# Performance work log

Hardware: AMD Instinct MI355X
Metric: run time of the kernel (lower is better)

Reference implementation:

```python
import jax, jax.numpy as jnp
import numpy as np

B, T, F, L = 512, 512, 128, 512  # batch, seq_len, n_features, latent_dim


def setup_inputs() -> dict:
    key = jax.random.key(0)
    ks = jax.random.split(key, 8)
    s = 1.0 / np.sqrt(L)  # torch default init scale for GRUCell (hidden_size=L)
    sd = 1.0 / np.sqrt(L)  # torch Linear(L, F) init scale
    return {
        "x": jax.random.normal(ks[0], (B, T, F), jnp.float32),
        "h_0": jax.random.normal(ks[1], (1, B, L), jnp.float32),
        "W_ih": jax.random.uniform(ks[2], (3 * L, F), jnp.float32, -s, s),
        "W_hh": jax.random.uniform(ks[3], (3 * L, L), jnp.float32, -s, s),
        "b_ih": jax.random.uniform(ks[4], (3 * L,), jnp.float32, -s, s),
        "b_hh": jax.random.uniform(ks[5], (3 * L,), jnp.float32, -s, s),
        "Wd": jax.random.uniform(ks[6], (F, L), jnp.float32, -sd, sd),
        "bd": jax.random.uniform(ks[7], (F,), jnp.float32, -sd, sd),
        "seq_len": T,
    }


def reference(x, h_0, W_ih, W_hh, b_ih, b_hh, Wd, bd, seq_len):
    # epsilon=0.0 default: teacher forcing never fires, so x_t = dense(h_t).
    h = jnp.squeeze(h_0, axis=0)          # [B, L]
    xt = h @ Wd.T + bd                    # [B, F]  (initial dense(h_0))

    def step(carry, _):
        h, xt = carry
        gi = xt @ W_ih.T + b_ih           # [B, 3L]
        gh = h @ W_hh.T + b_hh            # [B, 3L]
        i_r, i_z, i_n = jnp.split(gi, 3, axis=-1)
        h_r, h_z, h_n = jnp.split(gh, 3, axis=-1)
        r = jax.nn.sigmoid(i_r + h_r)
        z = jax.nn.sigmoid(i_z + h_z)
        n = jnp.tanh(i_n + r * h_n)
        h_new = (1.0 - z) * n + z * h     # [B, L]
        x_new = h_new @ Wd.T + bd         # [B, F] == dense(h_t) == output[:, t]
        return (h_new, x_new), x_new

    _, ys = jax.lax.scan(step, (h, xt), None, length=seq_len)  # ys: [T, B, F]
    return jnp.transpose(ys, (1, 0, 2))   # [B, T, F]
```

## Files before the change

kernel.cpp:

```cpp
#include <hip/hip_runtime.h>
#include <stdint.h>

typedef _Float16 f16;
typedef _Float16 half8 __attribute__((ext_vector_type(8)));
typedef _Float16 half4 __attribute__((ext_vector_type(4)));
typedef float float4v __attribute__((ext_vector_type(4)));
typedef float float2v __attribute__((ext_vector_type(2)));
typedef unsigned int u32;

#define MFMA16(A, B, C) __builtin_amdgcn_mfma_f32_16x16x32_f16((A), (B), (C), 0, 0, 0)

static constexpr int Bsz = 512, Tsz = 512, Fsz = 128, Lsz = 512;
static constexpr int NPACK = 2176;
static constexpr float LO_S = 2048.0f, LO_R = 1.0f / 2048.0f;

static constexpr size_t WSZ_FRAG  = (size_t)(NPACK / 16) * 16 * 64 * 8 * 2;
static constexpr size_t OFF_WHI   = 0;
static constexpr size_t OFF_WLO   = OFF_WHI + WSZ_FRAG;
static constexpr size_t OFF_BIAS  = OFF_WLO + WSZ_FRAG;
static constexpr size_t OFF_HHI   = OFF_BIAS + 16384;
static constexpr size_t OFF_HLO   = OFF_HHI + (size_t)2 * Bsz * Lsz * 2;
static constexpr size_t OFF_FLAGS = OFF_HLO + (size_t)2 * Bsz * Lsz * 2;

static constexpr int EXS = 37;
static constexpr int LDS_HI = 0;
static constexpr int LDS_LO = 32768;
static constexpr int LDS_EX = 65536;
static constexpr int LDS_YP = LDS_EX + 16 * 32 * EXS * 4;
static constexpr int LDS_TOT = LDS_YP + 4 * 32 * 17 * 4;

__device__ __host__ __forceinline__ int swz(int c, int r) {
  return (((c >> 3) ^ (r & 7)) << 3) | (c & 7);
}

__device__ __forceinline__ void async16(const void* g, void* l) {
  __builtin_amdgcn_global_load_lds((const __attribute__((address_space(1))) u32*)g,
                                   (__attribute__((address_space(3))) u32*)l, 16, 0, 16);
}

__device__ __forceinline__ float sigm(float x) { return 1.0f / (1.0f + __expf(-x)); }
__device__ __forceinline__ float tanh_(float x) { return 1.0f - 2.0f / (__expf(2.0f * x) + 1.0f); }

__global__ void k_pack(const float* __restrict__ Wih, const float* __restrict__ Whh,
                       const float* __restrict__ Wd, f16* __restrict__ whiF,
                       f16* __restrict__ wloF) {
  const int c = blockIdx.y;
  const int l = blockIdx.x * 256 + threadIdx.x;
  float v;
  if (c < 1536) {
    const float* wih = Wih + c * 128;
    float acc = 0.f;
#pragma unroll 8
    for (int f = 0; f < 128; ++f) acc = fmaf(Wd[f * 512 + l], wih[f], acc);
    v = acc;
    if (c < 1024) v += Whh[c * 512 + l];
  } else if (c < 2048) {
    v = Whh[(c - 512) * 512 + l];
  } else {
    v = Wd[(c - 2048) * 512 + l];
  }
  f16 hi = (f16)v;
  f16 lo = (f16)((v - (float)hi) * LO_S);
  const int chunk = c >> 4, ks = l >> 5, q = (l >> 3) & 3, j = l & 7, n = c & 15;
  const size_t idx = (((size_t)(chunk * 16 + ks)) * 64 + q * 16 + n) * 8 + j;
  whiF[idx] = hi;
  wloF[idx] = lo;
}

__global__ void k_init(const float* __restrict__ h0, const float* __restrict__ Wih,
                       const float* __restrict__ bih, const float* __restrict__ bhh,
                       const float* __restrict__ bd, f16* __restrict__ hhi,
                       f16* __restrict__ hlo, float* __restrict__ biasP,
                       int* __restrict__ flags) {
  const int t = blockIdx.x * 256 + threadIdx.x;
  if (t < Bsz * Lsz) {
    const int row = t >> 9, col = t & 511;
    float v = h0[t];
    f16 hi = (f16)v;
    f16 lo = (f16)((v - (float)hi) * LO_S);
    const int cp = swz(col, row);
    hhi[row * 512 + cp] = hi;
    hlo[row * 512 + cp] = lo;
  }
  if (t < NPACK) {
    float v;
    if (t < 1536) {
      float a = bih[t];
      for (int f = 0; f < 128; ++f) a = fmaf(Wih[t * 128 + f], bd[f], a);
      if (t < 1024) a += bhh[t];
      v = a;
    } else if (t < 2048) {
      v = bhh[t - 512];
    } else {
      v = bd[t - 2048];
    }
    biasP[t] = v;
  }
  if (t < 8192) flags[t] = 0;
}

__global__ __launch_bounds__(256, 1) void k_main(
    const float* __restrict__ h0, const f16* __restrict__ whiF,
    const f16* __restrict__ wloF, const float* __restrict__ biasP,
    f16* __restrict__ hhi, f16* __restrict__ hlo, int* __restrict__ flags,
    float* __restrict__ out) {
  extern __shared__ char dsm[];
  f16* sHi = (f16*)(dsm + LDS_HI);
  f16* sLo = (f16*)(dsm + LDS_LO);
  float* ex = (float*)(dsm + LDS_EX);
  float* yp = (float*)(dsm + LDS_YP);

  const int bid = blockIdx.x;
  const int g = bid & 15;
  const int m = bid >> 4;
  const int tid = threadIdx.x;
  const int v = tid >> 6, lane = tid & 63, q = lane >> 4, n = lane & 15;

  const half8* whiV = (const half8*)whiF;
  const half8* wloV = (const half8*)wloF;
  half8 w_hi[4][2][4], w_lo[4][2][4];
#pragma unroll
  for (int t = 0; t < 4; ++t)
#pragma unroll
    for (int nt = 0; nt < 2; ++nt)
#pragma unroll
      for (int ks = 0; ks < 4; ++ks) {
        const int idx = ((t * 32 + m * 2 + nt) * 16 + v * 4 + ks) * 64 + lane;
        w_hi[t][nt][ks] = whiV[idx];
        w_lo[t][nt][ks] = wloV[idx];
      }
  half8 w_y[4];
  if (m < 8) {
#pragma unroll
    for (int ks = 0; ks < 4; ++ks) w_y[ks] = whiV[((128 + m) * 16 + v * 4 + ks) * 64 + lane];
  }

  const int rl = tid >> 3, c0 = (tid & 7) * 4;
  float bias[4][4];
#pragma unroll
  for (int t = 0; t < 4; ++t)
#pragma unroll
    for (int cc = 0; cc < 4; ++cc) bias[t][cc] = biasP[t * 512 + m * 32 + c0 + cc];
  float hreg[4];
#pragma unroll
  for (int cc = 0; cc < 4; ++cc)
    hreg[cc] = h0[(size_t)(32 * g + rl) * 512 + m * 32 + c0 + cc];
  const int c2 = (tid & 7) * 2;
  float by[2] = {0.f, 0.f};
  if (m < 8) {
    by[0] = biasP[2048 + m * 16 + c2];
    by[1] = biasP[2048 + m * 16 + c2 + 1];
  }

  int* gcnt = flags + g * 64;
  const size_t rowbaseB = (size_t)(32 * g) * 1024;

  for (int s = 1; s <= 513; ++s) {
    {
      const char* srcHi = (const char*)hhi + (size_t)((s - 1) & 1) * 524288 + rowbaseB;
      const char* srcLo = (const char*)hlo + (size_t)((s - 1) & 1) * 524288 + rowbaseB;
      const int off = v * 8192 + lane * 16;
#pragma unroll
      for (int i = 0; i < 8; ++i) {
        async16(srcHi + off + i * 1024, dsm + LDS_HI + off + i * 1024);
        async16(srcLo + off + i * 1024, dsm + LDS_LO + off + i * 1024);
      }
    }
    __syncthreads();

    float4v yac[2];
    if (m < 8) { yac[0] = (float4v){0,0,0,0}; yac[1] = (float4v){0,0,0,0}; }
#pragma unroll
    for (int p = 0; p < 2; ++p) {
      float4v a_hh[2][2][2], a_ll[2][2][2];
#pragma unroll
      for (int ti = 0; ti < 2; ++ti)
#pragma unroll
        for (int nt = 0; nt < 2; ++nt)
#pragma unroll
          for (int mt = 0; mt < 2; ++mt) {
            a_hh[ti][nt][mt] = (float4v){0,0,0,0};
            a_ll[ti][nt][mt] = (float4v){0,0,0,0};
          }
#pragma unroll
      for (int ks = 0; ks < 4; ++ks) {
        half8 ah[2], al[2];
#pragma unroll
        for (int mt = 0; mt < 2; ++mt) {
          const int offE = (mt * 16 + n) * 512 + ((((v * 4 + ks) * 4 + q) ^ (n & 7)) * 8);
          ah[mt] = *(const half8*)(sHi + offE);
          al[mt] = *(const half8*)(sLo + offE);
        }
#pragma unroll
        for (int ti = 0; ti < 2; ++ti) {
          const int t = p * 2 + ti;
#pragma unroll
          for (int nt = 0; nt < 2; ++nt)
#pragma unroll
            for (int mt = 0; mt < 2; ++mt) {
              a_hh[ti][nt][mt] = MFMA16(ah[mt], w_hi[t][nt][ks], a_hh[ti][nt][mt]);
              a_ll[ti][nt][mt] = MFMA16(al[mt], w_hi[t][nt][ks], a_ll[ti][nt][mt]);
              a_ll[ti][nt][mt] = MFMA16(ah[mt], w_lo[t][nt][ks], a_ll[ti][nt][mt]);
            }
        }
        if (p == 0 && m < 8) {
          yac[0] = MFMA16(ah[0], w_y[ks], yac[0]);
          yac[1] = MFMA16(ah[1], w_y[ks], yac[1]);
        }
      }
#pragma unroll
      for (int ti = 0; ti < 2; ++ti) {
        const int t = p * 2 + ti;
#pragma unroll
        for (int nt = 0; nt < 2; ++nt)
#pragma unroll
          for (int mt = 0; mt < 2; ++mt) {
            const int base = ((t * 4 + v) * 32 + nt * 16 + n) * EXS + mt * 16 + q * 4;
            const float4v vv = a_hh[ti][nt][mt] + a_ll[ti][nt][mt] * LO_R;
            *(float2v*)(ex + base) = (float2v){vv[0], vv[1]};
            *(float2v*)(ex + base + 2) = (float2v){vv[2], vv[3]};
          }
      }
      if (p == 0 && m < 8) {
#pragma unroll
        for (int mt = 0; mt < 2; ++mt)
#pragma unroll
          for (int e = 0; e < 4; ++e)
            yp[(v * 32 + mt * 16 + q * 4 + e) * 17 + n] = yac[mt][e];
      }
    }
    __syncthreads();

    float pre[4][4];
#pragma unroll
    for (int t = 0; t < 4; ++t)
#pragma unroll
      for (int cc = 0; cc < 4; ++cc) {
        float acc = bias[t][cc];
#pragma unroll
        for (int w = 0; w < 4; ++w) acc += ex[((t * 4 + w) * 32 + c0 + cc) * EXS + rl];
        pre[t][cc] = acc;
      }
    const int rg = 32 * g + rl;
    half4 hiv, lov;
#pragma unroll
    for (int cc = 0; cc < 4; ++cc) {
      const float r = sigm(pre[0][cc]);
      const float z = sigm(pre[1][cc]);
      const float nn = tanh_(fmaf(r, pre[3][cc], pre[2][cc]));
      const float hn = fmaf(z, hreg[cc] - nn, nn);
      hreg[cc] = hn;
      const f16 hi = (f16)hn;
      hiv[cc] = hi;
      lov[cc] = (f16)((hn - (float)hi) * LO_S);
    }
    {
      const int colp = swz(m * 32 + c0, rg);
      const size_t o = (size_t)(s & 1) * 262144 + (size_t)rg * 512 + colp;
      __hip_atomic_store((uint64_t*)(hhi + o), __builtin_bit_cast(uint64_t, hiv),
                         __ATOMIC_RELAXED, __HIP_MEMORY_SCOPE_AGENT);
      __hip_atomic_store((uint64_t*)(hlo + o), __builtin_bit_cast(uint64_t, lov),
                         __ATOMIC_RELAXED, __HIP_MEMORY_SCOPE_AGENT);
    }
    asm volatile("s_waitcnt vmcnt(0)" ::: "memory");
    __syncthreads();
    if (tid == 0)
      __hip_atomic_fetch_add(gcnt, 1, __ATOMIC_RELAXED, __HIP_MEMORY_SCOPE_AGENT);

    if (m < 8 && s >= 2) {
#pragma unroll
      for (int cc = 0; cc < 2; ++cc) {
        float yv = by[cc];
#pragma unroll
        for (int w = 0; w < 4; ++w) yv += yp[(w * 32 + rl) * 17 + c2 + cc];
        __builtin_nontemporal_store(
            yv, out + (size_t)rg * (Tsz * Fsz) + (size_t)(s - 2) * Fsz + m * 16 + c2 + cc);
      }
    }

    if (s < 513) {
      if (tid == 0) {
        while (__hip_atomic_load(gcnt, __ATOMIC_RELAXED, __HIP_MEMORY_SCOPE_AGENT) <
               16 * s)
          __builtin_amdgcn_s_sleep(2);
      }
      __syncthreads();
    }
  }
}

extern "C" void kernel_launch(void* const* d_in, const int* in_sizes, int n_in,
                              void* d_out, int out_size, void* d_ws, size_t ws_size,
                              hipStream_t stream) {
  (void)in_sizes; (void)n_in; (void)out_size; (void)ws_size;
  const float* h0  = (const float*)d_in[1];
  const float* Wih = (const float*)d_in[2];
  const float* Whh = (const float*)d_in[3];
  const float* bih = (const float*)d_in[4];
  const float* bhh = (const float*)d_in[5];
  const float* Wd  = (const float*)d_in[6];
  const float* bd  = (const float*)d_in[7];
  float* out = (float*)d_out;
  char* ws = (char*)d_ws;

  f16* whiF    = (f16*)(ws + OFF_WHI);
  f16* wloF    = (f16*)(ws + OFF_WLO);
  float* biasP = (float*)(ws + OFF_BIAS);
  f16* hhi     = (f16*)(ws + OFF_HHI);
  f16* hlo     = (f16*)(ws + OFF_HLO);
  int* flags   = (int*)(ws + OFF_FLAGS);

  hipFuncSetAttribute((const void*)k_main, hipFuncAttributeMaxDynamicSharedMemorySize,
                      LDS_TOT);
  k_pack<<<dim3(2, NPACK), 256, 0, stream>>>(Wih, Whh, Wd, whiF, wloF);
  k_init<<<1024, 256, 0, stream>>>(h0, Wih, bih, bhh, bd, hhi, hlo, biasP, flags);
  k_main<<<256, 256, LDS_TOT, stream>>>(h0, whiF, wloF, biasP, hhi, hlo, flags, out);
}
```

Baseline: 4.599 ms.

## Add XCD-local fast path with workgroup-scope flags when a group shares an XCD

At launch each block records its XCC id and a nonce. At step two, tid 0 checks whether all 16 blocks in its batch group sit on the same XCD. If they do, the group switches to workgroup-scope stores, a second counter, and a different cache-policy bit on the async LDS loads, aiming for cheaper synchronisation than agent scope. The slow agent-scope stores and counter are kept as a fallback, so every step now writes h twice and adds barriers. Correctness relies on assumptions about L2 coherence within an XCD, and a spin timeout falls back to the old path.

```diff
diff --git a/kernel.cpp b/kernel.cpp
--- a/kernel.cpp
+++ b/kernel.cpp
@@ -22,12 +22,15 @@
 static constexpr size_t OFF_HLO   = OFF_HHI + (size_t)2 * Bsz * Lsz * 2;
 static constexpr size_t OFF_FLAGS = OFF_HLO + (size_t)2 * Bsz * Lsz * 2;
 
+static constexpr int NONCE = 0x5EED5EED;
+
 static constexpr int EXS = 37;
 static constexpr int LDS_HI = 0;
 static constexpr int LDS_LO = 32768;
 static constexpr int LDS_EX = 65536;
 static constexpr int LDS_YP = LDS_EX + 16 * 32 * EXS * 4;
-static constexpr int LDS_TOT = LDS_YP + 4 * 32 * 17 * 4;
+static constexpr int LDS_PROBE = LDS_YP + 4 * 32 * 17 * 4;
+static constexpr int LDS_TOT = LDS_PROBE + 16;
 
 __device__ __host__ __forceinline__ int swz(int c, int r) {
   return (((c >> 3) ^ (r & 7)) << 3) | (c & 7);
@@ -36,6 +39,10 @@
 __device__ __forceinline__ void async16(const void* g, void* l) {
   __builtin_amdgcn_global_load_lds((const __attribute__((address_space(1))) u32*)g,
                                    (__attribute__((address_space(3))) u32*)l, 16, 0, 16);
+}
+__device__ __forceinline__ void async16_l2(const void* g, void* l) {
+  __builtin_amdgcn_global_load_lds((const __attribute__((address_space(1))) u32*)g,
+                                   (__attribute__((address_space(3))) u32*)l, 16, 0, 1);
 }
 
 __device__ __forceinline__ float sigm(float x) { return 1.0f / (1.0f + __expf(-x)); }
@@ -116,6 +123,17 @@
   const int tid = threadIdx.x;
   const int v = tid >> 6, lane = tid & 63, q = lane >> 4, n = lane & 15;
 
+  int* xcds = flags + 2048;
+  int* nonc = flags + 4096;
+  int myxcc = 0;
+  if (tid == 0) {
+    myxcc = __builtin_amdgcn_s_getreg(6164);
+    __hip_atomic_store(nonc + bid * 16, NONCE, __ATOMIC_RELAXED,
+                       __HIP_MEMORY_SCOPE_WORKGROUP);
+    __hip_atomic_store(xcds + bid, myxcc, __ATOMIC_RELAXED, __HIP_MEMORY_SCOPE_AGENT);
+    *(int*)(dsm + LDS_PROBE) = 0;
+  }
+
   const half8* whiV = (const half8*)whiF;
   const half8* wloV = (const half8*)wloF;
   half8 w_hi[4][2][4], w_lo[4][2][4];
@@ -152,18 +170,41 @@
     by[1] = biasP[2048 + m * 16 + c2 + 1];
   }
 
-  int* gcnt = flags + g * 64;
+  int* gcnt  = flags + g * 64;
+  int* gcnt2 = flags + 1024 + g * 64;
+  int useL2r = 0;
   const size_t rowbaseB = (size_t)(32 * g) * 1024;
 
   for (int s = 1; s <= 513; ++s) {
+    if (s == 2 && tid == 0) {
+      int ok = 1;
+#pragma unroll 1
+      for (int mm = 0; mm < 16; ++mm) {
+        const int pb = mm * 16 + g;
+        ok &= (__hip_atomic_load(xcds + pb, __ATOMIC_RELAXED,
+                                 __HIP_MEMORY_SCOPE_AGENT) == myxcc);
+        ok &= (__hip_atomic_load(nonc + pb * 16, __ATOMIC_RELAXED,
+                                 __HIP_MEMORY_SCOPE_WORKGROUP) == NONCE);
+      }
+      *(int*)(dsm + LDS_PROBE) = ok;
+    }
+
     {
       const char* srcHi = (const char*)hhi + (size_t)((s - 1) & 1) * 524288 + rowbaseB;
       const char* srcLo = (const char*)hlo + (size_t)((s - 1) & 1) * 524288 + rowbaseB;
       const int off = v * 8192 + lane * 16;
-#pragma unroll
-      for (int i = 0; i < 8; ++i) {
-        async16(srcHi + off + i * 1024, dsm + LDS_HI + off + i * 1024);
-        async16(srcLo + off + i * 1024, dsm + LDS_LO + off + i * 1024);
+      if (useL2r) {
+#pragma unroll
+        for (int i = 0; i < 8; ++i) {
+          async16_l2(srcHi + off + i * 1024, dsm + LDS_HI + off + i * 1024);
+          async16_l2(srcLo + off + i * 1024, dsm + LDS_LO + off + i * 1024);
+        }
+      } else {
+#pragma unroll
+        for (int i = 0; i < 8; ++i) {
+          async16(srcHi + off + i * 1024, dsm + LDS_HI + off + i * 1024);
+          async16(srcLo + off + i * 1024, dsm + LDS_LO + off + i * 1024);
+        }
       }
     }
     __syncthreads();
@@ -254,14 +295,24 @@
       hiv[cc] = hi;
       lov[cc] = (f16)((hn - (float)hi) * LO_S);
     }
-    {
-      const int colp = swz(m * 32 + c0, rg);
-      const size_t o = (size_t)(s & 1) * 262144 + (size_t)rg * 512 + colp;
-      __hip_atomic_store((uint64_t*)(hhi + o), __builtin_bit_cast(uint64_t, hiv),
-                         __ATOMIC_RELAXED, __HIP_MEMORY_SCOPE_AGENT);
-      __hip_atomic_store((uint64_t*)(hlo + o), __builtin_bit_cast(uint64_t, lov),
-                         __ATOMIC_RELAXED, __HIP_MEMORY_SCOPE_AGENT);
-    }
+    const int colp = swz(m * 32 + c0, rg);
+    const size_t o = (size_t)(s & 1) * 262144 + (size_t)rg * 512 + colp;
+    const uint64_t H = __builtin_bit_cast(uint64_t, hiv);
+    const uint64_t L = __builtin_bit_cast(uint64_t, lov);
+
+    __hip_atomic_store((uint64_t*)(hhi + o), H, __ATOMIC_RELAXED,
+                       __HIP_MEMORY_SCOPE_WORKGROUP);
+    __hip_atomic_store((uint64_t*)(hlo + o), L, __ATOMIC_RELAXED,
+                       __HIP_MEMORY_SCOPE_WORKGROUP);
+    asm volatile("s_waitcnt vmcnt(0)" ::: "memory");
+    __syncthreads();
+    if (tid == 0)
+      __hip_atomic_fetch_add(gcnt2, 1, __ATOMIC_RELAXED, __HIP_MEMORY_SCOPE_WORKGROUP);
+
+    __hip_atomic_store((uint64_t*)(hhi + o), H, __ATOMIC_RELAXED,
+                       __HIP_MEMORY_SCOPE_AGENT);
+    __hip_atomic_store((uint64_t*)(hlo + o), L, __ATOMIC_RELAXED,
+                       __HIP_MEMORY_SCOPE_AGENT);
     asm volatile("s_waitcnt vmcnt(0)" ::: "memory");
     __syncthreads();
     if (tid == 0)
@@ -280,11 +331,27 @@
 
     if (s < 513) {
       if (tid == 0) {
-        while (__hip_atomic_load(gcnt, __ATOMIC_RELAXED, __HIP_MEMORY_SCOPE_AGENT) <
-               16 * s)
-          __builtin_amdgcn_s_sleep(2);
+        int u2 = useL2r;
+        if (u2) {
+          int spins = 0;
+          while (__hip_atomic_fetch_add(gcnt2, 0, __ATOMIC_RELAXED,
+                                        __HIP_MEMORY_SCOPE_WORKGROUP) < 16 * s) {
+            __builtin_amdgcn_s_sleep(1);
+            if (++spins > 20000) {
+              *(int*)(dsm + LDS_PROBE) = 0;
+              u2 = 0;
+              break;
+            }
+          }
+        }
+        if (!u2) {
+          while (__hip_atomic_load(gcnt, __ATOMIC_RELAXED, __HIP_MEMORY_SCOPE_AGENT) <
+                 16 * s)
+            __builtin_amdgcn_s_sleep(2);
+        }
       }
       __syncthreads();
+      useL2r = *(int*)(dsm + LDS_PROBE);
     }
   }
 }
```

Result: slower. 7.412 ms (+61.2%).
